# Optimization experiments

Hardware: AMD Instinct MI355X
Metric: run time of the kernel (lower is better)

## Reference

```python
import jax, jax.numpy as jnp
import numpy as np

NUM_BINS = 16
PADDING = 2.0


def _spline(u):
    # third-order (cubic B-spline) Parzen window kernel
    au = jnp.abs(u)
    su = au * au
    r1 = (4.0 - 6.0 * su + 3.0 * su * au) / 6.0          # |u| < 1
    r2 = (8.0 - 12.0 * au + 6.0 * su - su * au) / 6.0    # 1 <= |u| < 2
    return jnp.where(au < 1.0, r1, jnp.where(au < 2.0, r2, jnp.zeros_like(u)))


def setup_inputs() -> dict:
    key = jax.random.key(0)
    k1, k2 = jax.random.split(key)
    shape = (4, 1, 128, 128, 128)
    moving = jax.random.uniform(k1, shape, dtype=jnp.float32)
    fixed = jax.random.uniform(k2, shape, dtype=jnp.float32)
    return {"moving": moving, "fixed": fixed}


def reference(moving, fixed):
    nb = NUM_BINS
    B = moving.shape[0]
    m = moving.reshape(B, -1)
    f = fixed.reshape(B, -1)
    N = m.shape[1]

    fmin = f.min(1, keepdims=True); fmax = f.max(1, keepdims=True)
    mmin = m.min(1, keepdims=True); mmax = m.max(1, keepdims=True)
    fbs = (fmax - fmin) / (nb - 2.0 * PADDING)
    mbs = (mmax - mmin) / (nb - 2.0 * PADDING)

    # winTerm >= PADDING = 2, so int-truncation == floor
    f_term = f / fbs - (fmin / fbs - PADDING)
    m_term = m / mbs - (mmin / mbs - PADDING)
    f_idx = jnp.clip(f_term.astype(jnp.int32), 2, nb - 3)   # [B, N]
    m_idx = jnp.clip(m_term.astype(jnp.int32), 2, nb - 3)   # [B, N]

    b_off = jnp.arange(B, dtype=jnp.int32)[:, None]

    # joint histogram: 4-tap cubic spline scatter-add along the moving axis
    joint = jnp.zeros((B * nb * nb,), dtype=m.dtype)
    for off in (-1, 0, 1, 2):
        a = _spline((m_idx + off).astype(m_term.dtype) - m_term)  # [B, N]
        seg = (b_off * (nb * nb) + f_idx * nb + (m_idx + off)).ravel()
        joint = joint + jax.ops.segment_sum(a.ravel(), seg, num_segments=B * nb * nb)
    joint = joint.reshape(B, nb, nb)

    fixed_counts = jax.ops.segment_sum(
        jnp.ones((B * N,), dtype=m.dtype),
        (b_off * nb + f_idx).ravel(),
        num_segments=B * nb,
    ).reshape(B, nb)
    fixedPDF = fixed_counts / N                       # [B, nb]

    joint_norm = joint / joint.sum((1, 2), keepdims=True)   # [B, nb, nb]
    movingPDF = joint_norm.sum(1)                           # [B, nb]

    def plogp(p):
        return jnp.where(p > 0, p * jnp.log(jnp.where(p > 0, p, 1.0)), jnp.zeros_like(p))

    mi = plogp(joint_norm).sum((1, 2)) - plogp(movingPDF).sum(1) - plogp(fixedPDF).sum(1)
    return -jnp.mean(mi)
```

## Files before the change

kernel.cpp:

```cpp
#include <hip/hip_runtime.h>

#define NB 16
#define BATCHES 4
#define GX 32
#define BT 1024

typedef unsigned long long ull;

struct WS {
    float4 slot[BATCHES * GX];
    ull joint[BATCHES * 256];
    unsigned int fcount[BATCHES * NB];
};

__global__ __launch_bounds__(BT) void k_minmax(const float4* __restrict__ mov,
                                               const float4* __restrict__ fix,
                                               WS* __restrict__ ws, int nvec) {
    int t = threadIdx.x;
    int b = blockIdx.y, bx = blockIdx.x;
    if (bx == 0 && b == 0) {
        if (t < BATCHES * 256) ws->joint[t] = 0ull;
        if (t < BATCHES * NB) ws->fcount[t] = 0u;
    }
    const float4* m4 = mov + (size_t)b * nvec;
    const float4* f4 = fix + (size_t)b * nvec;
    int T = gridDim.x * BT;
    int i = bx * BT + t;
    float fmn = 3.4e38f, fmx = -3.4e38f, mmn = 3.4e38f, mmx = -3.4e38f;
    for (; i + 3 * T < nvec; i += 4 * T) {
        float4 f0 = f4[i], f1 = f4[i + T], f2 = f4[i + 2 * T], f3 = f4[i + 3 * T];
        float4 m0 = m4[i], m1 = m4[i + T], m2 = m4[i + 2 * T], m3 = m4[i + 3 * T];
        fmn = fminf(fmn, fminf(fminf(fminf(f0.x, f0.y), fminf(f0.z, f0.w)),
                               fminf(fminf(f1.x, f1.y), fminf(f1.z, f1.w))));
        fmn = fminf(fmn, fminf(fminf(fminf(f2.x, f2.y), fminf(f2.z, f2.w)),
                               fminf(fminf(f3.x, f3.y), fminf(f3.z, f3.w))));
        fmx = fmaxf(fmx, fmaxf(fmaxf(fmaxf(f0.x, f0.y), fmaxf(f0.z, f0.w)),
                               fmaxf(fmaxf(f1.x, f1.y), fmaxf(f1.z, f1.w))));
        fmx = fmaxf(fmx, fmaxf(fmaxf(fmaxf(f2.x, f2.y), fmaxf(f2.z, f2.w)),
                               fmaxf(fmaxf(f3.x, f3.y), fmaxf(f3.z, f3.w))));
        mmn = fminf(mmn, fminf(fminf(fminf(m0.x, m0.y), fminf(m0.z, m0.w)),
                               fminf(fminf(m1.x, m1.y), fminf(m1.z, m1.w))));
        mmn = fminf(mmn, fminf(fminf(fminf(m2.x, m2.y), fminf(m2.z, m2.w)),
                               fminf(fminf(m3.x, m3.y), fminf(m3.z, m3.w))));
        mmx = fmaxf(mmx, fmaxf(fmaxf(fmaxf(m0.x, m0.y), fmaxf(m0.z, m0.w)),
                               fmaxf(fmaxf(m1.x, m1.y), fmaxf(m1.z, m1.w))));
        mmx = fmaxf(mmx, fmaxf(fmaxf(fmaxf(m2.x, m2.y), fmaxf(m2.z, m2.w)),
                               fmaxf(fmaxf(m3.x, m3.y), fmaxf(m3.z, m3.w))));
    }
    for (; i < nvec; i += T) {
        float4 f = f4[i];
        float4 m = m4[i];
        fmn = fminf(fmn, fminf(fminf(f.x, f.y), fminf(f.z, f.w)));
        fmx = fmaxf(fmx, fmaxf(fmaxf(f.x, f.y), fmaxf(f.z, f.w)));
        mmn = fminf(mmn, fminf(fminf(m.x, m.y), fminf(m.z, m.w)));
        mmx = fmaxf(mmx, fmaxf(fmaxf(m.x, m.y), fmaxf(m.z, m.w)));
    }
    for (int d = 32; d; d >>= 1) {
        fmn = fminf(fmn, __shfl_xor(fmn, d));
        fmx = fmaxf(fmx, __shfl_xor(fmx, d));
        mmn = fminf(mmn, __shfl_xor(mmn, d));
        mmx = fmaxf(mmx, __shfl_xor(mmx, d));
    }
    __shared__ float4 wred[16];
    int wid = t >> 6, lane = t & 63;
    if (lane == 0) wred[wid] = make_float4(fmn, fmx, mmn, mmx);
    __syncthreads();
    if (wid == 0) {
        float4 s = wred[lane & 15];
        for (int d = 8; d; d >>= 1) {
            s.x = fminf(s.x, __shfl_xor(s.x, d));
            s.y = fmaxf(s.y, __shfl_xor(s.y, d));
            s.z = fminf(s.z, __shfl_xor(s.z, d));
            s.w = fmaxf(s.w, __shfl_xor(s.w, d));
        }
        if (lane == 0) ws->slot[b * GX + bx] = s;
    }
}

__global__ __launch_bounds__(BT) void k_hist(const float4* __restrict__ mov,
                                             const float4* __restrict__ fix,
                                             WS* __restrict__ ws, int nvec) {
    __shared__ ull ldsJ[8][256];
    __shared__ unsigned int ldsF[16][NB];
    __shared__ float4 mmbc;
    int t = threadIdx.x;
    int b = blockIdx.y, bx = blockIdx.x;

    for (int i = t; i < 8 * 256; i += BT) ((ull*)ldsJ)[i] = 0ull;
    if (t < 16 * NB) ((unsigned int*)ldsF)[t] = 0u;

    if (t < 64) {
        float4 s = ws->slot[b * GX + (t & (GX - 1))];
        for (int d = 32; d; d >>= 1) {
            s.x = fminf(s.x, __shfl_xor(s.x, d));
            s.y = fmaxf(s.y, __shfl_xor(s.y, d));
            s.z = fminf(s.z, __shfl_xor(s.z, d));
            s.w = fmaxf(s.w, __shfl_xor(s.w, d));
        }
        if (t == 0) mmbc = s;
    }
    __syncthreads();

    float fbs = (mmbc.y - mmbc.x) / 12.0f;
    float mbs = (mmbc.w - mmbc.z) / 12.0f;
    float fsh = mmbc.x / fbs - 2.0f;
    float msh = mmbc.z / mbs - 2.0f;

    int copy = t >> 7;
    int wid = t >> 6;
    const float4* m4 = mov + (size_t)b * nvec;
    const float4* f4 = fix + (size_t)b * nvec;
    int T = gridDim.x * BT;

    auto proc = [&](float fv, float mv) {
        float fterm = fv / fbs - fsh;
        int fi = (int)fterm;
        fi = fi < 2 ? 2 : (fi > NB - 3 ? NB - 3 : fi);
        float mterm = mv / mbs - msh;
        int mi_ = (int)mterm;
        mi_ = mi_ < 2 ? 2 : (mi_ > NB - 3 ? NB - 3 : mi_);
        atomicAdd(&ldsF[wid][fi], 1u);
        float b0 = (float)(mi_ - 1) - mterm;
        int baseIdx = fi * NB + mi_ - 1;
#pragma unroll
        for (int k = 0; k < 4; k++) {
            float u = b0 + (float)k;
            float au = fabsf(u);
            float su = au * au;
            float w;
            if (au < 1.0f)
                w = (4.0f - 6.0f * su + 3.0f * su * au) * (1.0f / 6.0f);
            else if (au < 2.0f)
                w = (8.0f - 12.0f * au + 6.0f * su - su * au) * (1.0f / 6.0f);
            else
                w = 0.0f;
            w = fmaxf(w, 0.0f);
            ull q = (ull)((double)w * 4294967296.0);
            atomicAdd(&ldsJ[copy][baseIdx + k], q);
        }
    };

    int i = bx * BT + t;
    for (; i + T < nvec; i += 2 * T) {
        float4 f0 = f4[i], f1 = f4[i + T];
        float4 m0 = m4[i], m1 = m4[i + T];
        proc(f0.x, m0.x); proc(f0.y, m0.y); proc(f0.z, m0.z); proc(f0.w, m0.w);
        proc(f1.x, m1.x); proc(f1.y, m1.y); proc(f1.z, m1.z); proc(f1.w, m1.w);
    }
    for (; i < nvec; i += T) {
        float4 fv = f4[i];
        float4 mv = m4[i];
        proc(fv.x, mv.x); proc(fv.y, mv.y); proc(fv.z, mv.z); proc(fv.w, mv.w);
    }
    __syncthreads();

    if (t < 256) {
        ull v = 0;
#pragma unroll
        for (int c = 0; c < 8; c++) v += ldsJ[c][t];
        if (v) atomicAdd(&ws->joint[b * 256 + t], v);
    } else if (t < 256 + NB) {
        int f = t - 256;
        unsigned int c = 0;
#pragma unroll
        for (int w = 0; w < 16; w++) c += ldsF[w][f];
        if (c) atomicAdd(&ws->fcount[b * NB + f], c);
    }
}

__global__ __launch_bounds__(1024) void k_final(const WS* __restrict__ ws,
                                                float* __restrict__ out, double invN) {
    __shared__ double shp[1024];
    __shared__ double red[1024];
    int t = threadIdx.x;
    int b = t >> 8;
    int bin = t & 255;

    double jt = (double)ws->joint[b * 256 + bin];
    red[t] = jt;
    __syncthreads();
    for (int s = 128; s > 0; s >>= 1) {
        if (bin < s) red[t] += red[t + s];
        __syncthreads();
    }
    double total = red[b * 256];
    __syncthreads();

    double p = jt / total;
    shp[t] = p;
    __syncthreads();

    double val = (p > 0.0) ? p * log(p) : 0.0;
    if (bin < NB) {
        double mp = 0.0;
        for (int f = 0; f < NB; f++) mp += shp[b * 256 + f * NB + bin];
        if (mp > 0.0) val -= mp * log(mp);
        double fp = (double)ws->fcount[b * NB + bin] * invN;
        if (fp > 0.0) val -= fp * log(fp);
    }
    __syncthreads();
    red[t] = val;
    __syncthreads();
    for (int s = 128; s > 0; s >>= 1) {
        if (bin < s) red[t] += red[t + s];
        __syncthreads();
    }
    if (t == 0) {
        double acc = red[0] + red[256] + red[512] + red[768];
        out[0] = (float)(-acc / (double)BATCHES);
    }
}

extern "C" void kernel_launch(void* const* d_in, const int* in_sizes, int n_in,
                              void* d_out, int out_size, void* d_ws, size_t ws_size,
                              hipStream_t stream) {
    const float* mov = (const float*)d_in[0];
    const float* fix = (const float*)d_in[1];
    float* out = (float*)d_out;
    WS* ws = (WS*)d_ws;

    int total = in_sizes[0];
    int N = total / BATCHES;
    int nvec = N / 4;

    dim3 grid(GX, BATCHES);
    k_minmax<<<grid, BT, 0, stream>>>((const float4*)mov, (const float4*)fix, ws, nvec);
    k_hist<<<grid, BT, 0, stream>>>((const float4*)mov, (const float4*)fix, ws, nvec);
    k_final<<<1, 1024, 0, stream>>>(ws, out, 1.0 / (double)N);
}
```

Baseline: 149.7 us.

## Rework histogram: more blocks, per-wave LDS copies, bank-swizzled bins, closed-form weights

Raises the grid from 32 to 128 blocks per batch and gives each wavefront its own LDS joint-histogram copy with a rotated (swizzled) column layout to cut atomic contention and bank conflicts. The spline weights are now computed directly from the fractional part (with w2 derived from partition of unity), and divisions become FMA with reciprocals. The separate fixed-count histogram is dropped: the fixed marginal is derived from joint row sums, and the final kernel is shrunk to 256 threads. Risks include small numeric differences from reciprocal multiplication and from 32-bit fixed-point truncation of the weights, and relies on row sums of the joint matching fixed counts.

```diff
diff --git a/kernel.cpp b/kernel.cpp
--- a/kernel.cpp
+++ b/kernel.cpp
@@ -2,7 +2,7 @@
 
 #define NB 16
 #define BATCHES 4
-#define GX 32
+#define GX 128
 #define BT 1024
 
 typedef unsigned long long ull;
@@ -10,7 +10,6 @@
 struct WS {
     float4 slot[BATCHES * GX];
     ull joint[BATCHES * 256];
-    unsigned int fcount[BATCHES * NB];
 };
 
 __global__ __launch_bounds__(BT) void k_minmax(const float4* __restrict__ mov,
@@ -18,10 +17,8 @@
                                                WS* __restrict__ ws, int nvec) {
     int t = threadIdx.x;
     int b = blockIdx.y, bx = blockIdx.x;
-    if (bx == 0 && b == 0) {
-        if (t < BATCHES * 256) ws->joint[t] = 0ull;
-        if (t < BATCHES * NB) ws->fcount[t] = 0u;
-    }
+    if (bx == 0 && b == 0) ws->joint[t] = 0ull;
+
     const float4* m4 = mov + (size_t)b * nvec;
     const float4* f4 = fix + (size_t)b * nvec;
     int T = gridDim.x * BT;
@@ -80,17 +77,20 @@
 __global__ __launch_bounds__(BT) void k_hist(const float4* __restrict__ mov,
                                              const float4* __restrict__ fix,
                                              WS* __restrict__ ws, int nvec) {
-    __shared__ ull ldsJ[8][256];
-    __shared__ unsigned int ldsF[16][NB];
+    __shared__ ull ldsJ[16][256];
     __shared__ float4 mmbc;
     int t = threadIdx.x;
     int b = blockIdx.y, bx = blockIdx.x;
-
-    for (int i = t; i < 8 * 256; i += BT) ((ull*)ldsJ)[i] = 0ull;
-    if (t < 16 * NB) ((unsigned int*)ldsF)[t] = 0u;
+    int wid = t >> 6;
+
+    #pragma unroll
+    for (int i = 0; i < 4; i++) ((ull*)ldsJ)[t + i * BT] = 0ull;
 
     if (t < 64) {
-        float4 s = ws->slot[b * GX + (t & (GX - 1))];
+        float4 a = ws->slot[b * GX + t];
+        float4 c = ws->slot[b * GX + t + 64];
+        float4 s = make_float4(fminf(a.x, c.x), fmaxf(a.y, c.y),
+                               fminf(a.z, c.z), fmaxf(a.w, c.w));
         for (int d = 32; d; d >>= 1) {
             s.x = fminf(s.x, __shfl_xor(s.x, d));
             s.y = fmaxf(s.y, __shfl_xor(s.y, d));
@@ -101,43 +101,39 @@
     }
     __syncthreads();
 
-    float fbs = (mmbc.y - mmbc.x) / 12.0f;
-    float mbs = (mmbc.w - mmbc.z) / 12.0f;
-    float fsh = mmbc.x / fbs - 2.0f;
-    float msh = mmbc.z / mbs - 2.0f;
-
-    int copy = t >> 7;
-    int wid = t >> 6;
+    float fbs = (mmbc.y - mmbc.x) * (1.0f / 12.0f);
+    float mbs = (mmbc.w - mmbc.z) * (1.0f / 12.0f);
+    float finv = 1.0f / fbs;
+    float minv = 1.0f / mbs;
+    float fofs = __builtin_fmaf(-mmbc.x, finv, 2.0f);
+    float mofs = __builtin_fmaf(-mmbc.z, minv, 2.0f);
+
+    ull* myJ = &ldsJ[wid][0];
     const float4* m4 = mov + (size_t)b * nvec;
     const float4* f4 = fix + (size_t)b * nvec;
     int T = gridDim.x * BT;
 
     auto proc = [&](float fv, float mv) {
-        float fterm = fv / fbs - fsh;
+        float fterm = __builtin_fmaf(fv, finv, fofs);
         int fi = (int)fterm;
         fi = fi < 2 ? 2 : (fi > NB - 3 ? NB - 3 : fi);
-        float mterm = mv / mbs - msh;
+        float mterm = __builtin_fmaf(mv, minv, mofs);
         int mi_ = (int)mterm;
         mi_ = mi_ < 2 ? 2 : (mi_ > NB - 3 ? NB - 3 : mi_);
-        atomicAdd(&ldsF[wid][fi], 1u);
-        float b0 = (float)(mi_ - 1) - mterm;
-        int baseIdx = fi * NB + mi_ - 1;
-#pragma unroll
-        for (int k = 0; k < 4; k++) {
-            float u = b0 + (float)k;
-            float au = fabsf(u);
-            float su = au * au;
-            float w;
-            if (au < 1.0f)
-                w = (4.0f - 6.0f * su + 3.0f * su * au) * (1.0f / 6.0f);
-            else if (au < 2.0f)
-                w = (8.0f - 12.0f * au + 6.0f * su - su * au) * (1.0f / 6.0f);
-            else
-                w = 0.0f;
-            w = fmaxf(w, 0.0f);
-            ull q = (ull)((double)w * 4294967296.0);
-            atomicAdd(&ldsJ[copy][baseIdx + k], q);
-        }
+        float tt = mterm - (float)mi_;
+        tt = fminf(fmaxf(tt, 0.0f), 1.0f);
+        float t2 = tt * tt;
+        float omt = 1.0f - tt;
+        float w0 = omt * omt * omt * (1.0f / 6.0f);
+        float w3 = tt * t2 * (1.0f / 6.0f);
+        float w1 = __builtin_fmaf(__builtin_fmaf(3.0f, tt, -6.0f), t2, 4.0f) * (1.0f / 6.0f);
+        float w2 = 1.0f - w0 - w1 - w3;
+        int row = fi << 4;
+        int s0 = (mi_ - 1 + 5 * fi) & 15;
+        atomicAdd(myJ + row + s0,             (ull)(unsigned int)(w0 * 4294967296.0f));
+        atomicAdd(myJ + row + ((s0 + 1) & 15), (ull)(unsigned int)(w1 * 4294967296.0f));
+        atomicAdd(myJ + row + ((s0 + 2) & 15), (ull)(unsigned int)(w2 * 4294967296.0f));
+        atomicAdd(myJ + row + ((s0 + 3) & 15), (ull)(unsigned int)(w3 * 4294967296.0f));
     };
 
     int i = bx * BT + t;
@@ -156,59 +152,53 @@
 
     if (t < 256) {
         ull v = 0;
-#pragma unroll
-        for (int c = 0; c < 8; c++) v += ldsJ[c][t];
+        #pragma unroll
+        for (int c = 0; c < 16; c++) v += ldsJ[c][t];
         if (v) atomicAdd(&ws->joint[b * 256 + t], v);
-    } else if (t < 256 + NB) {
-        int f = t - 256;
-        unsigned int c = 0;
-#pragma unroll
-        for (int w = 0; w < 16; w++) c += ldsF[w][f];
-        if (c) atomicAdd(&ws->fcount[b * NB + f], c);
-    }
-}
-
-__global__ __launch_bounds__(1024) void k_final(const WS* __restrict__ ws,
-                                                float* __restrict__ out, double invN) {
-    __shared__ double shp[1024];
-    __shared__ double red[1024];
-    int t = threadIdx.x;
-    int b = t >> 8;
-    int bin = t & 255;
-
-    double jt = (double)ws->joint[b * 256 + bin];
-    red[t] = jt;
-    __syncthreads();
-    for (int s = 128; s > 0; s >>= 1) {
-        if (bin < s) red[t] += red[t + s];
-        __syncthreads();
-    }
-    double total = red[b * 256];
-    __syncthreads();
-
-    double p = jt / total;
-    shp[t] = p;
-    __syncthreads();
-
-    double val = (p > 0.0) ? p * log(p) : 0.0;
-    if (bin < NB) {
-        double mp = 0.0;
-        for (int f = 0; f < NB; f++) mp += shp[b * 256 + f * NB + bin];
-        if (mp > 0.0) val -= mp * log(mp);
-        double fp = (double)ws->fcount[b * NB + bin] * invN;
-        if (fp > 0.0) val -= fp * log(fp);
-    }
-    __syncthreads();
-    red[t] = val;
-    __syncthreads();
-    for (int s = 128; s > 0; s >>= 1) {
-        if (bin < s) red[t] += red[t + s];
-        __syncthreads();
-    }
-    if (t == 0) {
-        double acc = red[0] + red[256] + red[512] + red[768];
-        out[0] = (float)(-acc / (double)BATCHES);
-    }
+    }
+}
+
+__global__ __launch_bounds__(256) void k_final(const WS* __restrict__ ws,
+                                               float* __restrict__ out) {
+    __shared__ double shp[256];
+    __shared__ double wsum[4];
+    int t = threadIdx.x, lane = t & 63, wid = t >> 6;
+    double acc = 0.0;
+    for (int b = 0; b < BATCHES; ++b) {
+        ull q = ws->joint[b * 256 + t];
+        double v = (double)q;
+        double s = v;
+        for (int d = 32; d; d >>= 1) s += __shfl_xor(s, d);
+        if (lane == 0) wsum[wid] = s;
+        __syncthreads();
+        double total = wsum[0] + wsum[1] + wsum[2] + wsum[3];
+        double p = v / total;
+        int f = t >> 4, c = t & 15, m = (c - 5 * f) & 15;
+        __syncthreads();
+        shp[f * 16 + m] = p;
+        double val = (q != 0ull) ? p * log(p) : 0.0;
+        __syncthreads();
+        if (t < 16) {
+            double mp = 0.0;
+            #pragma unroll
+            for (int f2 = 0; f2 < 16; ++f2) mp += shp[f2 * 16 + t];
+            if (mp > 0.0) val -= mp * log(mp);
+        } else if (t < 32) {
+            int f2 = t - 16;
+            double fp = 0.0;
+            #pragma unroll
+            for (int m2 = 0; m2 < 16; ++m2) fp += shp[f2 * 16 + m2];
+            if (fp > 0.0) val -= fp * log(fp);
+        }
+        double s2 = val;
+        for (int d = 32; d; d >>= 1) s2 += __shfl_xor(s2, d);
+        __syncthreads();
+        if (lane == 0) wsum[wid] = s2;
+        __syncthreads();
+        if (t == 0) acc += wsum[0] + wsum[1] + wsum[2] + wsum[3];
+        __syncthreads();
+    }
+    if (t == 0) out[0] = (float)(-acc / (double)BATCHES);
 }
 
 extern "C" void kernel_launch(void* const* d_in, const int* in_sizes, int n_in,
@@ -226,5 +216,5 @@
     dim3 grid(GX, BATCHES);
     k_minmax<<<grid, BT, 0, stream>>>((const float4*)mov, (const float4*)fix, ws, nvec);
     k_hist<<<grid, BT, 0, stream>>>((const float4*)mov, (const float4*)fix, ws, nvec);
-    k_final<<<1, 1024, 0, stream>>>(ws, out, 1.0 / (double)N);
-}
+    k_final<<<1, 256, 0, stream>>>(ws, out);
+}
```

New measurement: 121.5 us. -18.8%, faster.
